# Kernel tuning notes

Measured on AMD Instinct MI355X. Metric: run time of the kernel, lower is better.

## Reference

```python
import jax, jax.numpy as jnp
import numpy as np

NUM_HEADS = 16
D_MODEL = 1024
NEG_INF = -1e30


def setup_inputs() -> dict:
    key = jax.random.key(0)
    ks = jax.random.split(key, 7)
    B, S, D = 2, 2048, D_MODEL
    scale = 1.0 / np.sqrt(D)
    return {
        "queries": jax.random.normal(ks[0], (B, S, D), dtype=jnp.float32),
        "keys": jax.random.normal(ks[1], (B, S, D), dtype=jnp.float32),
        "values": jax.random.normal(ks[2], (B, S, D), dtype=jnp.float32),
        "Wq": jax.random.normal(ks[3], (D, D), dtype=jnp.float32) * scale,
        "Wk": jax.random.normal(ks[4], (D, D), dtype=jnp.float32) * scale,
        "Wv": jax.random.normal(ks[5], (D, D), dtype=jnp.float32) * scale,
        "Wo": jax.random.normal(ks[6], (D, D), dtype=jnp.float32) * scale,
    }


def _split_heads(x, h):
    # [B, S, D] -> [B, h, S, D/h]
    B, S, D = x.shape
    return x.reshape(B, S, h, D // h).transpose(0, 2, 1, 3)


def reference(queries, keys, values, Wq, Wk, Wv, Wo):
    h = NUM_HEADS
    q = _split_heads(queries @ Wq, h)  # [B, h, S, dh]
    k = _split_heads(keys @ Wk, h)
    v = _split_heads(values @ Wv, h)
    dh = q.shape[-1]
    scores = jnp.einsum("bhqd,bhkd->bhqk", q, k) / jnp.sqrt(jnp.float32(dh))
    # original quirk: exactly-zero scores are masked to -1e30 before softmax
    scores = jnp.where(scores == 0, NEG_INF, scores)
    attn = jax.nn.softmax(scores, axis=-1)
    out = jnp.einsum("bhqk,bhkd->bhqd", attn, v)  # [B, h, S, dh]
    B, _, S, _ = out.shape
    out = out.transpose(0, 2, 1, 3).reshape(B, S, h * dh)
    return out @ Wo
```

## Files before the change

### kernel.cpp

```cpp
#include <hip/hip_runtime.h>

typedef unsigned short u16;
typedef short bf16x8 __attribute__((ext_vector_type(8)));
typedef float f32x4 __attribute__((ext_vector_type(4)));
typedef float f32x16 __attribute__((ext_vector_type(16)));

namespace {

constexpr int kB = 2, kS = 2048, kD = 1024, kH = 16, kDh = 64;
constexpr float kC2 = 0.125f * 1.44269504088896341f;

__device__ inline u16 f32_bf16(float f) {
    unsigned u = __float_as_uint(f);
    u += 0x7FFFu + ((u >> 16) & 1u);
    return (u16)(u >> 16);
}

__device__ inline float fast_exp2(float x) {
    float r;
    asm("v_exp_f32 %0, %1" : "=v"(r) : "v"(x));
    return r;
}

__device__ inline unsigned cvtpk(float a, float b) {
    unsigned r;
    asm("v_cvt_pk_bf16_f32 %0, %1, %2" : "=v"(r) : "v"(a), "v"(b));
    return r;
}

__device__ inline void plswap(unsigned& a, unsigned& b) {
    asm("v_permlane32_swap_b32 %0, %1" : "+v"(a), "+v"(b));
}

__device__ inline void gl_lds16(const void* g, void* l) {
    __builtin_amdgcn_global_load_lds(
        (const __attribute__((address_space(1))) void*)g,
        (__attribute__((address_space(3))) void*)l, 16, 0, 0);
}

__device__ inline int swz8(int l) {
    return ((l & 3) ^ ((l >> 2) & 3) ^ ((l >> 4) & 3)) * 8;
}

__global__ __launch_bounds__(256) void prep(
    const float* __restrict__ s0, const float* __restrict__ s1,
    const float* __restrict__ s2,
    u16* __restrict__ d0, u16* __restrict__ d1, u16* __restrict__ d2,
    const float* __restrict__ W0, const float* __restrict__ W1,
    const float* __restrict__ W2, const float* __restrict__ W3,
    u16* __restrict__ T0, u16* __restrict__ T1,
    u16* __restrict__ T2, u16* __restrict__ T3)
{
    const int y = blockIdx.y;
    if (y < 3) {
        const float* src = y == 0 ? s0 : (y == 1 ? s1 : s2);
        u16* dst = y == 0 ? d0 : (y == 1 ? d1 : d2);
        const int i = blockIdx.x * 256 + threadIdx.x;
        const float4* s4 = (const float4*)src;
        float4 a = s4[2 * i], b = s4[2 * i + 1];
        uint4 o;
        o.x = (unsigned)f32_bf16(a.x) | ((unsigned)f32_bf16(a.y) << 16);
        o.y = (unsigned)f32_bf16(a.z) | ((unsigned)f32_bf16(a.w) << 16);
        o.z = (unsigned)f32_bf16(b.x) | ((unsigned)f32_bf16(b.y) << 16);
        o.w = (unsigned)f32_bf16(b.z) | ((unsigned)f32_bf16(b.w) << 16);
        ((uint4*)dst)[i] = o;
        return;
    }
    if (blockIdx.x >= 256) return;
    const int z = y - 3;
    const float* W = z == 0 ? W0 : (z == 1 ? W1 : (z == 2 ? W2 : W3));
    u16* Wt = z == 0 ? T0 : (z == 1 ? T1 : (z == 2 ? T2 : T3));
    const float sc = (z == 0) ? kC2 : 1.0f;

    __shared__ __attribute__((aligned(16))) u16 T[64][65];
    const int t = threadIdx.x;
    const int n0 = (blockIdx.x & 15) * 64, k0 = (blockIdx.x >> 4) * 64;
    const int r = t >> 4, c4 = (t & 15) * 4;
#pragma unroll
    for (int it = 0; it < 4; ++it) {
        const int rr = r + 16 * it;
        float4 v = *(const float4*)(W + (size_t)(k0 + rr) * kD + n0 + c4);
        T[rr][c4 + 0] = f32_bf16(v.x * sc);
        T[rr][c4 + 1] = f32_bf16(v.y * sc);
        T[rr][c4 + 2] = f32_bf16(v.z * sc);
        T[rr][c4 + 3] = f32_bf16(v.w * sc);
    }
    __syncthreads();
#pragma unroll
    for (int it = 0; it < 4; ++it) {
        const int nn = r + 16 * it;
        uint2 pk;
        pk.x = (unsigned)T[c4 + 0][nn] | ((unsigned)T[c4 + 1][nn] << 16);
        pk.y = (unsigned)T[c4 + 2][nn] | ((unsigned)T[c4 + 3][nn] << 16);
        *(uint2*)(Wt + (size_t)(n0 + nn) * kD + k0 + c4) = pk;
    }
}

__global__ __launch_bounds__(256) void vtrans(
    const u16* __restrict__ V, u16* __restrict__ Vt)
{
    __shared__ __attribute__((aligned(16))) u16 T[64][65];
    const int t = threadIdx.x;
    const int s0 = blockIdx.x * 64;
    const int bh = blockIdx.y, b = bh >> 4, h = bh & 15;
    const int rr = t >> 3, c0 = (t & 7) * 8;
    union { u16 u[8]; uint4 v4; } buf;
#pragma unroll
    for (int p = 0; p < 2; ++p) {
        const int s = rr + 32 * p;
        buf.v4 = *(const uint4*)(V + (size_t)(b * kS + s0 + s) * kD + h * kDh + c0);
#pragma unroll
        for (int i = 0; i < 8; ++i) T[c0 + i][s] = buf.u[i];
    }
    __syncthreads();
#pragma unroll
    for (int p = 0; p < 2; ++p) {
        const int d = rr + 32 * p;
#pragma unroll
        for (int i = 0; i < 8; ++i) buf.u[i] = T[d][c0 + i];
        *(uint4*)(Vt + (size_t)(bh * kDh + d) * kS + s0 + c0) = buf.v4;
    }
}

template <bool F32OUT>
__device__ inline void gemm128_body(
    const u16* __restrict__ A, const u16* __restrict__ Wt,
    void* __restrict__ Cout, int M, int N, int K, int bx, int by)
{
    __shared__ __attribute__((aligned(16))) u16 As[128 * 32];
    __shared__ __attribute__((aligned(16))) u16 Bs[128 * 32];
    const int t = threadIdx.x, w = t >> 6, l = t & 63;
    const int quad = l >> 4, c = l & 15;
    const int wm = w >> 1, wn = w & 1;
    const int m0 = by * 128, n0 = bx * 128;
    const int lr = l >> 2, lc = swz8(l);
    const int xc = ((quad ^ (c & 3) ^ ((c >> 2) & 3))) * 8;

    const u16* ga0 = A  + (size_t)(m0 + w * 32 + lr) * K + lc;
    const u16* ga1 = A  + (size_t)(m0 + w * 32 + 16 + lr) * K + lc;
    const u16* gb0 = Wt + (size_t)(n0 + w * 32 + lr) * K + lc;
    const u16* gb1 = Wt + (size_t)(n0 + w * 32 + 16 + lr) * K + lc;
    u16* la0 = &As[(w * 32) * 32];
    u16* la1 = &As[(w * 32 + 16) * 32];
    u16* lb0 = &Bs[(w * 32) * 32];
    u16* lb1 = &Bs[(w * 32 + 16) * 32];

    f32x4 acc[4][4];
#pragma unroll
    for (int mi = 0; mi < 4; ++mi)
#pragma unroll
        for (int nj = 0; nj < 4; ++nj) acc[mi][nj] = 0;

    for (int k0 = 0; k0 < K; k0 += 32) {
        gl_lds16(ga0 + k0, la0);
        gl_lds16(ga1 + k0, la1);
        gl_lds16(gb0 + k0, lb0);
        gl_lds16(gb1 + k0, lb1);
        __syncthreads();
        bf16x8 af[4], bf[4];
#pragma unroll
        for (int mi = 0; mi < 4; ++mi)
            af[mi] = *(const bf16x8*)&As[(wm * 64 + mi * 16 + c) * 32 + xc];
#pragma unroll
        for (int nj = 0; nj < 4; ++nj)
            bf[nj] = *(const bf16x8*)&Bs[(wn * 64 + nj * 16 + c) * 32 + xc];
#pragma unroll
        for (int mi = 0; mi < 4; ++mi)
#pragma unroll
            for (int nj = 0; nj < 4; ++nj)
                acc[mi][nj] = __builtin_amdgcn_mfma_f32_16x16x32_bf16(
                    af[mi], bf[nj], acc[mi][nj], 0, 0, 0);
        __syncthreads();
    }

#pragma unroll
    for (int mi = 0; mi < 4; ++mi)
#pragma unroll
        for (int nj = 0; nj < 4; ++nj)
#pragma unroll
            for (int r = 0; r < 4; ++r) {
                const size_t row = m0 + wm * 64 + mi * 16 + quad * 4 + r;
                const size_t col = n0 + wn * 64 + nj * 16 + c;
                if (F32OUT)
                    ((float*)Cout)[row * N + col] = acc[mi][nj][r];
                else
                    ((u16*)Cout)[row * N + col] = f32_bf16(acc[mi][nj][r]);
            }
}

__global__ __launch_bounds__(256) void gemm_qkv(
    const u16* __restrict__ A0, const u16* __restrict__ A1,
    const u16* __restrict__ A2,
    const u16* __restrict__ W0, const u16* __restrict__ W1,
    const u16* __restrict__ W2,
    u16* __restrict__ C0, u16* __restrict__ C1, u16* __restrict__ C2)
{
    const int z = blockIdx.z;
    const u16* A  = z == 0 ? A0 : (z == 1 ? A1 : A2);
    const u16* Wt = z == 0 ? W0 : (z == 1 ? W1 : W2);
    u16* C = z == 0 ? C0 : (z == 1 ? C1 : C2);
    gemm128_body<false>(A, Wt, C, kB * kS, kD, kD, blockIdx.x, blockIdx.y);
}

__global__ __launch_bounds__(256) void gemm_out(
    const u16* __restrict__ A, const u16* __restrict__ Wt,
    float* __restrict__ C)
{
    __shared__ __attribute__((aligned(16))) u16 As[64 * 32];
    __shared__ __attribute__((aligned(16))) u16 Bs[128 * 32];
    const int N = kD, K = kD;
    const int t = threadIdx.x, w = t >> 6, l = t & 63;
    const int quad = l >> 4, c = l & 15;
    const int wm = w >> 1, wn = w & 1;
    const int m0 = blockIdx.y * 64, n0 = blockIdx.x * 128;
    const int lr = l >> 2, lc = swz8(l);
    const int xc = ((quad ^ (c & 3) ^ ((c >> 2) & 3))) * 8;

    const u16* ga  = A  + (size_t)(m0 + w * 16 + lr) * K + lc;
    const u16* gb0 = Wt + (size_t)(n0 + w * 16 + lr) * K + lc;
    const u16* gb1 = Wt + (size_t)(n0 + 64 + w * 16 + lr) * K + lc;
    u16* la  = &As[(w * 16) * 32];
    u16* lb0 = &Bs[(w * 16) * 32];
    u16* lb1 = &Bs[(64 + w * 16) * 32];

    f32x4 acc[2][4];
#pragma unroll
    for (int mi = 0; mi < 2; ++mi)
#pragma unroll
        for (int nj = 0; nj < 4; ++nj) acc[mi][nj] = 0;

    for (int k0 = 0; k0 < K; k0 += 32) {
        gl_lds16(ga + k0, la);
        gl_lds16(gb0 + k0, lb0);
        gl_lds16(gb1 + k0, lb1);
        __syncthreads();
        bf16x8 af[2], bf[4];
#pragma unroll
        for (int mi = 0; mi < 2; ++mi)
            af[mi] = *(const bf16x8*)&As[(wm * 32 + mi * 16 + c) * 32 + xc];
#pragma unroll
        for (int nj = 0; nj < 4; ++nj)
            bf[nj] = *(const bf16x8*)&Bs[(wn * 64 + nj * 16 + c) * 32 + xc];
#pragma unroll
        for (int mi = 0; mi < 2; ++mi)
#pragma unroll
            for (int nj = 0; nj < 4; ++nj)
                acc[mi][nj] = __builtin_amdgcn_mfma_f32_16x16x32_bf16(
                    af[mi], bf[nj], acc[mi][nj], 0, 0, 0);
        __syncthreads();
    }

#pragma unroll
    for (int mi = 0; mi < 2; ++mi)
#pragma unroll
        for (int nj = 0; nj < 4; ++nj)
#pragma unroll
            for (int r = 0; r < 4; ++r) {
                const size_t row = m0 + wm * 32 + mi * 16 + quad * 4 + r;
                const size_t col = n0 + wn * 64 + nj * 16 + c;
                C[row * N + col] = acc[mi][nj][r];
            }
}

__global__ __launch_bounds__(256) void attn(
    const u16* __restrict__ Q, const u16* __restrict__ K,
    const u16* __restrict__ Vt, u16* __restrict__ AO)
{
    __shared__ __attribute__((aligned(16))) u16 KsA[64 * 64];
    __shared__ __attribute__((aligned(16))) u16 KsB[64 * 64];
    __shared__ __attribute__((aligned(16))) u16 VtA[64 * 64];
    __shared__ __attribute__((aligned(16))) u16 VtB[64 * 64];

    const int t = threadIdx.x, w = t >> 6, l = t & 63;
    const int half = l >> 5, m = l & 31;
    const int q0 = blockIdx.x * 128;
    const int bh = blockIdx.y, b = bh >> 4, h = bh & 15;
    const int sr = l >> 3;
    const int sc = (l & 7) ^ sr;

    const size_t kbase = (size_t)(b * kS) * kD + h * kDh;
    const size_t vbase = (size_t)bh * kDh * kS;

    auto stage = [&](int kt, u16* KsP, u16* VtP) {
#pragma unroll
        for (int i = 0; i < 2; ++i) {
            const int R0 = w * 16 + i * 8;
            gl_lds16(K + kbase + (size_t)(kt * 64 + R0 + sr) * kD + sc * 8,
                     &KsP[R0 * 64]);
            gl_lds16(Vt + vbase + (size_t)(R0 + sr) * kS + kt * 64 + sc * 8,
                     &VtP[R0 * 64]);
        }
    };

    stage(0, KsA, VtA);

    bf16x8 qf[4];
    {
        const u16* qp = Q + (size_t)(b * kS + q0 + w * 32 + m) * kD
                        + h * kDh + half * 8;
#pragma unroll
        for (int ch = 0; ch < 4; ++ch)
            qf[ch] = *(const bf16x8*)(qp + ch * 16);
    }

    bf16x8 ones;
#pragma unroll
    for (int i = 0; i < 8; ++i) ones[i] = (short)0x3F80;

    f32x16 o0 = 0, o1 = 0;
    f32x16 ol = 0;

    __syncthreads();

    auto compute = [&](const u16* KsP, const u16* VtP) {
        f32x16 s0 = 0, s1 = 0;
        __builtin_amdgcn_s_setprio(1);
#pragma unroll
        for (int ch = 0; ch < 4; ++ch) {
            const int xo = ((2 * ch + half) ^ (m & 7)) * 8;
            const bf16x8 kf0 = *(const bf16x8*)&KsP[(m) * 64 + xo];
            const bf16x8 kf1 = *(const bf16x8*)&KsP[(32 + m) * 64 + xo];
            s0 = __builtin_amdgcn_mfma_f32_32x32x16_bf16(kf0, qf[ch], s0, 0, 0, 0);
            s1 = __builtin_amdgcn_mfma_f32_32x32x16_bf16(kf1, qf[ch], s1, 0, 0, 0);
        }
        __builtin_amdgcn_s_setprio(0);
#pragma unroll
        for (int r = 0; r < 16; ++r) {
            s0[r] = fast_exp2(s0[r]);
            s1[r] = fast_exp2(s1[r]);
        }
        __builtin_amdgcn_s_setprio(1);
#pragma unroll
        for (int ts = 0; ts < 4; ++ts) {
            const int rb = (ts & 1) * 8;
            unsigned c0, c1, c2, c3;
            if (ts < 2) {
                c0 = cvtpk(s0[rb + 0], s0[rb + 1]);
                c1 = cvtpk(s0[rb + 2], s0[rb + 3]);
                c2 = cvtpk(s0[rb + 4], s0[rb + 5]);
                c3 = cvtpk(s0[rb + 6], s0[rb + 7]);
            } else {
                c0 = cvtpk(s1[rb + 0], s1[rb + 1]);
                c1 = cvtpk(s1[rb + 2], s1[rb + 3]);
                c2 = cvtpk(s1[rb + 4], s1[rb + 5]);
                c3 = cvtpk(s1[rb + 6], s1[rb + 7]);
            }
            plswap(c0, c2);
            plswap(c1, c3);
            union { unsigned u[4]; bf16x8 v; } pb;
            pb.u[0] = c0; pb.u[1] = c1; pb.u[2] = c2; pb.u[3] = c3;
            const int xo = ((2 * ts + half) ^ (m & 7)) * 8;
            const bf16x8 vf0 = *(const bf16x8*)&VtP[(m) * 64 + xo];
            const bf16x8 vf1 = *(const bf16x8*)&VtP[(32 + m) * 64 + xo];
            o0 = __builtin_amdgcn_mfma_f32_32x32x16_bf16(vf0, pb.v, o0, 0, 0, 0);
            o1 = __builtin_amdgcn_mfma_f32_32x32x16_bf16(vf1, pb.v, o1, 0, 0, 0);
            ol = __builtin_amdgcn_mfma_f32_32x32x16_bf16(ones, pb.v, ol, 0, 0, 0);
        }
        __builtin_amdgcn_s_setprio(0);
    };

    constexpr int NT = kS / 64;
#pragma unroll 1
    for (int kt = 0; kt < NT; kt += 2) {
        if (kt + 1 < NT) stage(kt + 1, KsB, VtB);
        compute(KsA, VtA);
        __syncthreads();
        if (kt + 2 < NT) stage(kt + 2, KsA, VtA);
        compute(KsB, VtB);
        __syncthreads();
    }

    const float inv = 1.0f / ol[0];

    u16* ob = w == 0 ? KsA : (w == 1 ? KsB : (w == 2 ? VtA : VtB));
#pragma unroll
    for (int r = 0; r < 4; ++r) {
        uint2 p0, p1;
        p0.x = cvtpk(o0[4 * r + 0] * inv, o0[4 * r + 1] * inv);
        p0.y = cvtpk(o0[4 * r + 2] * inv, o0[4 * r + 3] * inv);
        p1.x = cvtpk(o1[4 * r + 0] * inv, o1[4 * r + 1] * inv);
        p1.y = cvtpk(o1[4 * r + 2] * inv, o1[4 * r + 3] * inv);
        *(uint2*)&ob[m * 64 + ((r ^ (m & 7)) << 3) + 4 * half] = p0;
        *(uint2*)&ob[m * 64 + (((4 + r) ^ (m & 7)) << 3) + 4 * half] = p1;
    }
    const size_t obase = (size_t)(b * kS + q0 + w * 32) * kD + h * kDh;
#pragma unroll
    for (int i = 0; i < 4; ++i) {
        const int q = l >> 1;
        const int tt = (l & 1) + i * 2;
        uint4 dd = *(const uint4*)&ob[q * 64 + ((tt ^ (q & 7)) << 3)];
        *(uint4*)(AO + obase + (size_t)q * kD + tt * 8) = dd;
    }
}

}

extern "C" void kernel_launch(void* const* d_in, const int* in_sizes, int n_in,
                              void* d_out, int out_size, void* d_ws, size_t ws_size,
                              hipStream_t stream)
{
    const float* q_in = (const float*)d_in[0];
    const float* k_in = (const float*)d_in[1];
    const float* v_in = (const float*)d_in[2];
    const float* Wq   = (const float*)d_in[3];
    const float* Wk   = (const float*)d_in[4];
    const float* Wv   = (const float*)d_in[5];
    const float* Wo   = (const float*)d_in[6];

    u16* ws = (u16*)d_ws;
    const size_t M1 = 1u << 20;
    u16* xq  = ws;
    u16* xk  = ws + 4 * M1;
    u16* xv  = ws + 8 * M1;
    u16* Wtq = ws + 12 * M1;
    u16* Wtk = ws + 13 * M1;
    u16* Wtv = ws + 14 * M1;
    u16* Wto = ws + 15 * M1;
    u16* Qp  = ws + 16 * M1;
    u16* Kp  = ws + 20 * M1;
    u16* Vp  = ws + 24 * M1;
    u16* AO  = ws + 28 * M1;
    u16* Vtg = xq;

    hipLaunchKernelGGL(prep, dim3(2048, 7), dim3(256), 0, stream,
                       q_in, k_in, v_in, xq, xk, xv,
                       Wq, Wk, Wv, Wo, Wtq, Wtk, Wtv, Wto);

    hipLaunchKernelGGL(gemm_qkv, dim3(8, 32, 3), dim3(256), 0, stream,
                       xq, xk, xv, Wtq, Wtk, Wtv, Qp, Kp, Vp);

    hipLaunchKernelGGL(vtrans, dim3(32, 32), dim3(256), 0, stream, Vp, Vtg);

    hipLaunchKernelGGL(attn, dim3(16, 32), dim3(256), 0, stream, Qp, Kp, Vtg, AO);

    hipLaunchKernelGGL(gemm_out, dim3(8, 64), dim3(256), 0, stream,
                       AO, Wto, (float*)d_out);
}
```

Baseline: 218.6 us.

## Split attention over key halves with a separate combine kernel

Splits the attention kernel across two halves of the key sequence (grid z=2). Each half writes unnormalized partial outputs in fp16 plus its row sums to workspace, and a new combine kernel adds the partials, normalizes and converts to bf16. This doubles the attention grid from 512 to 1024 blocks to fill the GPU better. In exchange it adds an extra launch and extra memory traffic for the partials. The scheme relies on the softmax using a fixed max (no running max), so the partials can simply be summed, and fp16 partials risk overflow or precision loss.

```diff
diff --git a/kernel.cpp b/kernel.cpp
--- a/kernel.cpp
+++ b/kernel.cpp
@@ -25,6 +25,12 @@
 __device__ inline unsigned cvtpk(float a, float b) {
     unsigned r;
     asm("v_cvt_pk_bf16_f32 %0, %1, %2" : "=v"(r) : "v"(a), "v"(b));
+    return r;
+}
+
+__device__ inline unsigned pkf16(float a, float b) {
+    unsigned r;
+    asm("v_cvt_pkrtz_f16_f32 %0, %1, %2" : "=v"(r) : "v"(a), "v"(b));
     return r;
 }
 
@@ -264,7 +270,7 @@
 
 __global__ __launch_bounds__(256) void attn(
     const u16* __restrict__ Q, const u16* __restrict__ K,
-    const u16* __restrict__ Vt, u16* __restrict__ AO)
+    const u16* __restrict__ Vt, u16* __restrict__ PO, float* __restrict__ L)
 {
     __shared__ __attribute__((aligned(16))) u16 KsA[64 * 64];
     __shared__ __attribute__((aligned(16))) u16 KsB[64 * 64];
@@ -275,19 +281,21 @@
     const int half = l >> 5, m = l & 31;
     const int q0 = blockIdx.x * 128;
     const int bh = blockIdx.y, b = bh >> 4, h = bh & 15;
+    const int g = blockIdx.z;
     const int sr = l >> 3;
     const int sc = (l & 7) ^ sr;
 
     const size_t kbase = (size_t)(b * kS) * kD + h * kDh;
     const size_t vbase = (size_t)bh * kDh * kS;
+    const int kg0 = g * (kS / 2);
 
     auto stage = [&](int kt, u16* KsP, u16* VtP) {
 #pragma unroll
         for (int i = 0; i < 2; ++i) {
             const int R0 = w * 16 + i * 8;
-            gl_lds16(K + kbase + (size_t)(kt * 64 + R0 + sr) * kD + sc * 8,
+            gl_lds16(K + kbase + (size_t)(kg0 + kt * 64 + R0 + sr) * kD + sc * 8,
                      &KsP[R0 * 64]);
-            gl_lds16(Vt + vbase + (size_t)(R0 + sr) * kS + kt * 64 + sc * 8,
+            gl_lds16(Vt + vbase + (size_t)(R0 + sr) * kS + kg0 + kt * 64 + sc * 8,
                      &VtP[R0 * 64]);
         }
     };
@@ -359,7 +367,7 @@
         __builtin_amdgcn_s_setprio(0);
     };
 
-    constexpr int NT = kS / 64;
+    constexpr int NT = (kS / 2) / 64;
 #pragma unroll 1
     for (int kt = 0; kt < NT; kt += 2) {
         if (kt + 1 < NT) stage(kt + 1, KsB, VtB);
@@ -370,27 +378,53 @@
         __syncthreads();
     }
 
-    const float inv = 1.0f / ol[0];
-
     u16* ob = w == 0 ? KsA : (w == 1 ? KsB : (w == 2 ? VtA : VtB));
 #pragma unroll
     for (int r = 0; r < 4; ++r) {
         uint2 p0, p1;
-        p0.x = cvtpk(o0[4 * r + 0] * inv, o0[4 * r + 1] * inv);
-        p0.y = cvtpk(o0[4 * r + 2] * inv, o0[4 * r + 3] * inv);
-        p1.x = cvtpk(o1[4 * r + 0] * inv, o1[4 * r + 1] * inv);
-        p1.y = cvtpk(o1[4 * r + 2] * inv, o1[4 * r + 3] * inv);
+        p0.x = pkf16(o0[4 * r + 0], o0[4 * r + 1]);
+        p0.y = pkf16(o0[4 * r + 2], o0[4 * r + 3]);
+        p1.x = pkf16(o1[4 * r + 0], o1[4 * r + 1]);
+        p1.y = pkf16(o1[4 * r + 2], o1[4 * r + 3]);
         *(uint2*)&ob[m * 64 + ((r ^ (m & 7)) << 3) + 4 * half] = p0;
         *(uint2*)&ob[m * 64 + (((4 + r) ^ (m & 7)) << 3) + 4 * half] = p1;
     }
-    const size_t obase = (size_t)(b * kS + q0 + w * 32) * kD + h * kDh;
+    const size_t srow = (size_t)(g * 32 + bh) * kS + q0 + w * 32;
+    if (l < 32) L[srow + l] = ol[0];
 #pragma unroll
     for (int i = 0; i < 4; ++i) {
         const int q = l >> 1;
         const int tt = (l & 1) + i * 2;
         uint4 dd = *(const uint4*)&ob[q * 64 + ((tt ^ (q & 7)) << 3)];
-        *(uint4*)(AO + obase + (size_t)q * kD + tt * 8) = dd;
-    }
+        *(uint4*)(PO + (srow + q) * 64 + tt * 8) = dd;
+    }
+}
+
+__global__ __launch_bounds__(256) void combine(
+    const u16* __restrict__ PO, const float* __restrict__ L,
+    u16* __restrict__ AO)
+{
+    typedef _Float16 f16;
+    const size_t chunk = (size_t)blockIdx.x * 256 + threadIdx.x;
+    const size_t flat = chunk * 8;
+    const int bh = (int)(flat >> 17);
+    const int s  = (int)((flat >> 6) & 2047);
+    const int d  = (int)(flat & 63);
+    const float l0 = L[(size_t)bh * kS + s];
+    const float l1 = L[(size_t)(32 + bh) * kS + s];
+    const float inv = 1.0f / (l0 + l1);
+    union { uint4 v; f16 hx[8]; } a, c;
+    a.v = *(const uint4*)(PO + flat);
+    c.v = *(const uint4*)(PO + (size_t)(32) * kS * 64 + flat);
+    unsigned o[4];
+#pragma unroll
+    for (int j = 0; j < 4; ++j) {
+        const float x0 = ((float)a.hx[2 * j]     + (float)c.hx[2 * j])     * inv;
+        const float x1 = ((float)a.hx[2 * j + 1] + (float)c.hx[2 * j + 1]) * inv;
+        o[j] = (unsigned)f32_bf16(x0) | ((unsigned)f32_bf16(x1) << 16);
+    }
+    const int b = bh >> 4, h = bh & 15;
+    *(uint4*)(AO + ((size_t)(b * kS + s)) * kD + h * kDh + d) = *(uint4*)o;
 }
 
 }
@@ -421,6 +455,8 @@
     u16* Vp  = ws + 24 * M1;
     u16* AO  = ws + 28 * M1;
     u16* Vtg = xq;
+    u16* PO  = xk;
+    float* Lb = (float*)Vp;
 
     hipLaunchKernelGGL(prep, dim3(2048, 7), dim3(256), 0, stream,
                        q_in, k_in, v_in, xq, xk, xv,
@@ -431,7 +467,10 @@
 
     hipLaunchKernelGGL(vtrans, dim3(32, 32), dim3(256), 0, stream, Vp, Vtg);
 
-    hipLaunchKernelGGL(attn, dim3(16, 32), dim3(256), 0, stream, Qp, Kp, Vtg, AO);
+    hipLaunchKernelGGL(attn, dim3(16, 32, 2), dim3(256), 0, stream,
+                       Qp, Kp, Vtg, PO, Lb);
+
+    hipLaunchKernelGGL(combine, dim3(2048), dim3(256), 0, stream, PO, Lb, AO);
 
     hipLaunchKernelGGL(gemm_out, dim3(8, 64), dim3(256), 0, stream,
                        AO, Wto, (float*)d_out);
```

Measured after the change: 221.8 us. Within noise of the previous version (+1.4%).
